# Performance work log

Measured on AMD Instinct MI355X. Metric: run time of the kernel, lower is better.

The kernel has to match this reference:

```python
import jax, jax.numpy as jnp
import numpy as np

N = 50000
E = 1600000
IN = 128
HID = 32
HEADS = 4
SLOPE = 0.2   # GATConv default negative_slope
EPS = 1e-5    # BatchNorm eps


def setup_inputs() -> dict:
    key = jax.random.key(0)
    ks = jax.random.split(key, 16)
    inp = {}
    inp["x"] = jax.random.normal(ks[0], (N, IN), dtype=jnp.float32)
    inp["edge_index"] = jax.random.randint(ks[1], (2, E), 0, N, dtype=jnp.int32)
    def p(k, shape, s=0.1):
        return jax.random.normal(k, shape, dtype=jnp.float32) * s
    # layer dims: (in_ch, out_ch_per_head, heads, concat)
    dims = [(IN, HID, HEADS, True), (HID * HEADS, HID, HEADS, True), (HID * HEADS, HID, 1, False)]
    i = 2
    for li, (ic, oc, h, concat) in enumerate(dims):
        inp[f"W{li}"] = p(ks[i], (ic, h * oc)); i += 1
        inp[f"as{li}"] = p(ks[i], (h, oc)); i += 1
        inp[f"ad{li}"] = p(ks[i], (h, oc)); i += 1
        bn_dim = h * oc if concat else oc
        inp[f"b{li}"] = jnp.zeros((bn_dim,), jnp.float32)
        inp[f"g{li}"] = jnp.ones((bn_dim,), jnp.float32)
        inp[f"be{li}"] = jnp.zeros((bn_dim,), jnp.float32)
    inp["cw1"] = p(ks[i], (HID, HID // 2)); i += 1
    inp["cb1"] = jnp.zeros((HID // 2,), jnp.float32)
    inp["cw2"] = p(ks[i], (HID // 2, 2)); i += 1
    inp["cb2"] = jnp.zeros((2,), jnp.float32)
    return inp


def _gat_layer(h, src, dst, W, a_s, a_d, b, heads, oc, concat):
    # PyG GATConv: x -> [N,H,C]; alpha = softmax_dst(leaky_relu(a_s.x_src + a_d.x_dst))
    n = h.shape[0]
    x = (h @ W).reshape(n, heads, oc)                 # [N,H,C]
    e_s = (x * a_s).sum(-1)                            # [N,H]
    e_d = (x * a_d).sum(-1)                            # [N,H]
    e = jax.nn.leaky_relu(e_s[src] + e_d[dst], SLOPE)  # [Etot,H]
    m = jax.ops.segment_max(e, dst, num_segments=n)    # segment softmax over dst
    ex = jnp.exp(e - m[dst])
    den = jax.ops.segment_sum(ex, dst, num_segments=n)
    alpha = ex / (den[dst] + 1e-16)                    # [Etot,H]
    out = jax.ops.segment_sum(x[src] * alpha[:, :, None], dst, num_segments=n)  # [N,H,C]
    out = out.reshape(n, heads * oc) if concat else out.mean(1)
    return out + b


def _bn(x, g, be):
    mu = x.mean(0)
    var = x.var(0)  # biased, as torch BN uses for normalization
    return g * (x - mu) * jax.lax.rsqrt(var + EPS) + be


def reference(x, edge_index, W0, as0, ad0, b0, g0, be0, W1, as1, ad1, b1, g1, be1,
              W2, as2, ad2, b2, g2, be2, cw1, cb1, cw2, cb2):
    n = x.shape[0]
    loops = jnp.arange(n, dtype=edge_index.dtype)      # add_self_loops=True default
    src = jnp.concatenate([edge_index[0], loops])
    dst = jnp.concatenate([edge_index[1], loops])
    layers = [(W0, as0, ad0, b0, g0, be0, HEADS, HID, True),
              (W1, as1, ad1, b1, g1, be1, HEADS, HID, True),
              (W2, as2, ad2, b2, g2, be2, 1, HID, False)]
    h = x
    for (W, a_s, a_d, b, g, be, heads, oc, concat) in layers:
        h = _gat_layer(h, src, dst, W, a_s, a_d, b, heads, oc, concat)
        h = jax.nn.elu(_bn(h, g, be))
    h = jax.nn.elu(h @ cw1 + cb1)
    return h @ cw2 + cb2
```

## Files before the change

### kernel.cpp

```cpp
#include <hip/hip_runtime.h>

static constexpr float SLOPE = 0.2f;
static constexpr float BN_EPS = 1e-5f;

static inline int cdiv(long long a, long long b) { return (int)((a + b - 1) / b); }

typedef __attribute__((ext_vector_type(8))) short short8;
typedef __attribute__((ext_vector_type(4))) float f32x4;

__device__ __forceinline__ unsigned short f2bf(float f) {
  unsigned u = __float_as_uint(f);
  u += 0x7fff + ((u >> 16) & 1);
  return (unsigned short)(u >> 16);
}
__device__ __forceinline__ float bf2f(unsigned short h) {
  return __uint_as_float((unsigned)h << 16);
}

static constexpr int EPB = 16384;

__global__ void csr_hist(const int* __restrict__ ei, int* __restrict__ counts,
                         int E, int NBLK, int NB) {
  __shared__ int cnt[256];
  const int tid = threadIdx.x;
  cnt[tid] = 0;
  __syncthreads();
  const int i0 = blockIdx.x * EPB;
  const int i1 = min(E, i0 + EPB);
  for (int i = i0 + tid; i < i1; i += 256) {
    int d = ei[E + i];
    atomicAdd(&cnt[d >> 8], 1);
  }
  __syncthreads();
  if (tid < NB) counts[tid * NBLK + blockIdx.x] = cnt[tid];
}

__global__ void csr_scan(const int* __restrict__ counts, int* __restrict__ offsets, int m) {
  __shared__ int wtot[16];
  __shared__ int woff[17];
  __shared__ int carry_sh;
  const int tid = threadIdx.x;
  const int lane = tid & 63;
  const int wv = tid >> 6;
  if (tid == 0) carry_sh = 0;
  __syncthreads();
  for (int base = 0; base < m; base += 1024) {
    int i = base + tid;
    int v = (i < m) ? counts[i] : 0;
    int x = v;
#pragma unroll
    for (int off = 1; off < 64; off <<= 1) {
      int y = __shfl_up(x, off);
      if (lane >= off) x += y;
    }
    if (lane == 63) wtot[wv] = x;
    __syncthreads();
    if (tid == 0) {
      int r = 0;
#pragma unroll
      for (int w = 0; w < 16; ++w) { woff[w] = r; r += wtot[w]; }
      woff[16] = r;
    }
    __syncthreads();
    if (i < m) offsets[i] = x - v + woff[wv] + carry_sh;
    __syncthreads();
    if (tid == 0) carry_sh += woff[16];
    __syncthreads();
  }
  if (tid == 0) offsets[m] = carry_sh;
}

__global__ void csr_part(const int* __restrict__ ei, const int* __restrict__ offsets,
                         unsigned* __restrict__ ebuf, int E, int NBLK, int NB) {
  __shared__ int cur[256];
  const int tid = threadIdx.x;
  cur[tid] = (tid < NB) ? offsets[tid * NBLK + blockIdx.x] : 0;
  __syncthreads();
  const int i0 = blockIdx.x * EPB;
  const int i1 = min(E, i0 + EPB);
  for (int i = i0 + tid; i < i1; i += 256) {
    int s = ei[i];
    int d = ei[E + i];
    int p = atomicAdd(&cur[d >> 8], 1);
    ebuf[p] = ((unsigned)s << 8) | (unsigned)(d & 255);
  }
}

__global__ void csr_bucket(const unsigned* __restrict__ ebuf, const int* __restrict__ offsets,
                           int* __restrict__ row_start, int* __restrict__ csr_src,
                           int n, int E, int NBLK, int NB) {
  __shared__ int nstart[256];
  __shared__ int wtot[4];
  const int b = blockIdx.x;
  const int base = b << 8;
  const int nn = min(256, n - base);
  const int estart = offsets[b * NBLK];
  const int eend = (b + 1 < NB) ? offsets[(b + 1) * NBLK] : E;
  const int gstart = estart + base;
  const int tid = threadIdx.x;
  nstart[tid] = (tid < nn) ? 1 : 0;
  __syncthreads();
  for (int j = estart + tid; j < eend; j += 256) {
    atomicAdd(&nstart[ebuf[j] & 255u], 1);
  }
  __syncthreads();
  const int lane = tid & 63, wv = tid >> 6;
  int v = nstart[tid];
  int x = v;
#pragma unroll
  for (int off = 1; off < 64; off <<= 1) {
    int y = __shfl_up(x, off);
    if (lane >= off) x += y;
  }
  if (lane == 63) wtot[wv] = x;
  __syncthreads();
  int add = 0;
  for (int w = 0; w < wv; ++w) add += wtot[w];
  int excl = x - v + add;
  __syncthreads();
  nstart[tid] = excl;
  if (tid < nn) row_start[base + tid] = gstart + excl;
  if (b == 0 && tid == 0) row_start[n] = E + n;
  __syncthreads();
  if (tid < nn) {
    int p = atomicAdd(&nstart[tid], 1);
    csr_src[gstart + p] = base + tid;
  }
  for (int j = estart + tid; j < eend; j += 256) {
    unsigned pk = ebuf[j];
    int p = atomicAdd(&nstart[pk & 255u], 1);
    csr_src[gstart + p] = (int)(pk >> 8);
  }
}

__global__ void wprep(const float* __restrict__ W0, const float* __restrict__ W1,
                      const float* __restrict__ W2,
                      unsigned short* __restrict__ Wt0, unsigned short* __restrict__ Wt1,
                      unsigned short* __restrict__ Wt2,
                      float* __restrict__ sums0, float* __restrict__ sums1,
                      float* __restrict__ sums2) {
  const int b = blockIdx.x;
  const int tid = threadIdx.x;
  if (b < 64) {
    int o = b * 256 + tid;
    int j = o >> 7, k = o & 127;
    Wt0[o] = f2bf(W0[k * 128 + j]);
  } else if (b < 128) {
    int o = (b - 64) * 256 + tid;
    int j = o >> 7, k = o & 127;
    Wt1[o] = f2bf(W1[k * 128 + j]);
  } else if (b < 144) {
    int o = (b - 128) * 256 + tid;
    int j = o >> 7, k = o & 127;
    Wt2[o] = f2bf(W2[k * 32 + j]);
  } else {
    sums0[tid] = 0.f;
    sums1[tid] = 0.f;
    if (tid < 64) sums2[tid] = 0.f;
  }
}

template<int IC, int OC, int H, bool BN, bool AF32>
__global__ void gemm_mfma(const unsigned short* __restrict__ Act,
                          const float* __restrict__ Axf,
                          const unsigned short* __restrict__ Wt,
                          const float* __restrict__ a_s, const float* __restrict__ a_d,
                          const float* __restrict__ bnsums, const float* __restrict__ g,
                          const float* __restrict__ be,
                          unsigned short* __restrict__ Pb, float* __restrict__ es,
                          float* __restrict__ ed, int n) {
  constexpr int NF = OC / 16;
  __shared__ float s_sc[IC], s_sf[IC];
  const int tid = threadIdx.x;
  if (BN) {
    const float inv_n = 1.f / (float)n;
    for (int c = tid; c < IC; c += 256) {
      float mu = bnsums[c] * inv_n;
      float var = bnsums[IC + c] * inv_n - mu * mu;
      float s = g[c] * rsqrtf(var + BN_EPS);
      s_sc[c] = s;
      s_sf[c] = be[c] - mu * s;
    }
    __syncthreads();
  }
  const int lane = tid & 63;
  const int l15 = lane & 15;
  const int lk = lane >> 4;
  const int node0 = blockIdx.x * 64 + (tid >> 6) * 16;
  const int arow = node0 + l15;
  const int ar = AF32 ? min(arow, n - 1) : arow;

  f32x4 acc[NF];
#pragma unroll
  for (int cb = 0; cb < NF; ++cb) acc[cb] = (f32x4){0.f, 0.f, 0.f, 0.f};

#pragma unroll
  for (int kc = 0; kc < IC / 32; ++kc) {
    const int kbase = kc * 32 + lk * 8;
    short8 a;
    if (AF32) {
      float4 u0 = *(const float4*)(Axf + (size_t)ar * IC + kbase);
      float4 u1 = *(const float4*)(Axf + (size_t)ar * IC + kbase + 4);
      a[0] = (short)f2bf(u0.x); a[1] = (short)f2bf(u0.y);
      a[2] = (short)f2bf(u0.z); a[3] = (short)f2bf(u0.w);
      a[4] = (short)f2bf(u1.x); a[5] = (short)f2bf(u1.y);
      a[6] = (short)f2bf(u1.z); a[7] = (short)f2bf(u1.w);
    } else {
      a = *(const short8*)(Act + (size_t)ar * IC + kbase);
    }
    if (BN) {
      short8 ta;
#pragma unroll
      for (int i = 0; i < 8; ++i) {
        float v = bf2f((unsigned short)a[i]);
        float y = fmaf(v, s_sc[kbase + i], s_sf[kbase + i]);
        y = (y > 0.f) ? y : (__expf(y) - 1.f);
        ta[i] = (short)f2bf(y);
      }
      a = ta;
    }
#pragma unroll
    for (int cb = 0; cb < NF; ++cb) {
      short8 b = *(const short8*)(Wt + (size_t)(cb * 16 + l15) * IC + kbase);
      acc[cb] = __builtin_amdgcn_mfma_f32_16x16x32_bf16(a, b, acc[cb], 0, 0, 0);
    }
  }

  float esum[4] = {0.f, 0.f, 0.f, 0.f}, edum[4] = {0.f, 0.f, 0.f, 0.f};
#pragma unroll
  for (int cb = 0; cb < NF; ++cb) {
    const int j = cb * 16 + l15;
    const float asv = a_s[j];
    const float adv = a_d[j];
#pragma unroll
    for (int i = 0; i < 4; ++i) {
      float p = acc[cb][i];
      int node = node0 + lk * 4 + i;
      if (node < n) Pb[(size_t)node * OC + j] = f2bf(p);
      float ps = p * asv, pd = p * adv;
#pragma unroll
      for (int mm = 1; mm <= 8; mm <<= 1) {
        ps += __shfl_xor(ps, mm);
        pd += __shfl_xor(pd, mm);
      }
      esum[i] += ps;
      edum[i] += pd;
    }
    if (cb & 1) {
      const int h = cb >> 1;
#pragma unroll
      for (int i = 0; i < 4; ++i) {
        int node = node0 + lk * 4 + i;
        if (l15 == 0 && node < n) {
          es[node * H + h] = esum[i];
          ed[node * H + h] = edum[i];
        }
        esum[i] = 0.f;
        edum[i] = 0.f;
      }
    }
  }
}

template<int H, int C>
__global__ void node_agg(const int* __restrict__ row_start, const int* __restrict__ csr_src,
                         const float* __restrict__ es, const float* __restrict__ ed,
                         const unsigned short* __restrict__ Pb, unsigned short* __restrict__ Ob,
                         int n) {
  constexpr int HC = H * C;
  constexpr int TPN = HC / 8;
  const int tid = threadIdx.x;
  const int t = tid % TPN;
  const int node = blockIdx.x * (256 / TPN) + tid / TPN;
  if (node >= n) return;
  const int h = (t * 8) / C;
  const int e0 = row_start[node];
  const int e1 = row_start[node + 1];
  const float edd = ed[node * H + h];
  const uint4* P4 = (const uint4*)Pb;
  float a0 = 0.f, a1 = 0.f, a2 = 0.f, a3 = 0.f;
  float a4 = 0.f, a5 = 0.f, a6 = 0.f, a7 = 0.f;
  float den = 0.f;
  int s0 = csr_src[e0];
  int s1 = (e0 + 1 < e1) ? csr_src[e0 + 1] : 0;
  int j = e0;
  while (j + 1 < e1) {
    const int nj = j + 2;
    int t0 = (nj < e1) ? csr_src[nj] : 0;
    int t1 = (nj + 1 < e1) ? csr_src[nj + 1] : 0;
    float x0 = es[s0 * H + h], x1 = es[s1 * H + h];
    uint4 p0 = P4[(size_t)s0 * TPN + t];
    uint4 p1 = P4[(size_t)s1 * TPN + t];
    x0 += edd; x0 = fmaxf(x0, SLOPE * x0); float w0 = __expf(x0);
    x1 += edd; x1 = fmaxf(x1, SLOPE * x1); float w1 = __expf(x1);
    den += w0 + w1;
    a0 = fmaf(w0, __uint_as_float(p0.x << 16), a0);
    a1 = fmaf(w0, __uint_as_float(p0.x & 0xffff0000u), a1);
    a2 = fmaf(w0, __uint_as_float(p0.y << 16), a2);
    a3 = fmaf(w0, __uint_as_float(p0.y & 0xffff0000u), a3);
    a4 = fmaf(w0, __uint_as_float(p0.z << 16), a4);
    a5 = fmaf(w0, __uint_as_float(p0.z & 0xffff0000u), a5);
    a6 = fmaf(w0, __uint_as_float(p0.w << 16), a6);
    a7 = fmaf(w0, __uint_as_float(p0.w & 0xffff0000u), a7);
    a0 = fmaf(w1, __uint_as_float(p1.x << 16), a0);
    a1 = fmaf(w1, __uint_as_float(p1.x & 0xffff0000u), a1);
    a2 = fmaf(w1, __uint_as_float(p1.y << 16), a2);
    a3 = fmaf(w1, __uint_as_float(p1.y & 0xffff0000u), a3);
    a4 = fmaf(w1, __uint_as_float(p1.z << 16), a4);
    a5 = fmaf(w1, __uint_as_float(p1.z & 0xffff0000u), a5);
    a6 = fmaf(w1, __uint_as_float(p1.w << 16), a6);
    a7 = fmaf(w1, __uint_as_float(p1.w & 0xffff0000u), a7);
    s0 = t0; s1 = t1; j = nj;
  }
  if (j < e1) {
    float x0 = es[s0 * H + h] + edd;
    x0 = fmaxf(x0, SLOPE * x0);
    float w0 = __expf(x0);
    den += w0;
    uint4 p0 = P4[(size_t)s0 * TPN + t];
    a0 = fmaf(w0, __uint_as_float(p0.x << 16), a0);
    a1 = fmaf(w0, __uint_as_float(p0.x & 0xffff0000u), a1);
    a2 = fmaf(w0, __uint_as_float(p0.y << 16), a2);
    a3 = fmaf(w0, __uint_as_float(p0.y & 0xffff0000u), a3);
    a4 = fmaf(w0, __uint_as_float(p0.z << 16), a4);
    a5 = fmaf(w0, __uint_as_float(p0.z & 0xffff0000u), a5);
    a6 = fmaf(w0, __uint_as_float(p0.w << 16), a6);
    a7 = fmaf(w0, __uint_as_float(p0.w & 0xffff0000u), a7);
  }
  float inv = 1.f / (den + 1e-16f);
  uint4 o;
  o.x = (unsigned)f2bf(a0 * inv) | ((unsigned)f2bf(a1 * inv) << 16);
  o.y = (unsigned)f2bf(a2 * inv) | ((unsigned)f2bf(a3 * inv) << 16);
  o.z = (unsigned)f2bf(a4 * inv) | ((unsigned)f2bf(a5 * inv) << 16);
  o.w = (unsigned)f2bf(a6 * inv) | ((unsigned)f2bf(a7 * inv) << 16);
  *(uint4*)(Ob + (size_t)node * HC + t * 8) = o;
}

template<int C>
__global__ void bn_stats2(const unsigned short* __restrict__ X, float* __restrict__ sums,
                          int n) {
  constexpr int TPR = C / 4;
  constexpr int RPB = 256 / TPR;
  __shared__ float ls[2 * C];
  const int tid = threadIdx.x;
  for (int i = tid; i < 2 * C; i += 256) ls[i] = 0.f;
  __syncthreads();
  const int c4 = (tid % TPR) * 4;
  const int rb = tid / TPR;
  float s0 = 0.f, s1 = 0.f, s2 = 0.f, s3 = 0.f;
  float q0 = 0.f, q1 = 0.f, q2 = 0.f, q3 = 0.f;
  for (int r = blockIdx.x * RPB + rb; r < n; r += gridDim.x * RPB) {
    uint2 v = *(const uint2*)(X + (size_t)r * C + c4);
    float f0 = __uint_as_float(v.x << 16);
    float f1 = __uint_as_float(v.x & 0xffff0000u);
    float f2 = __uint_as_float(v.y << 16);
    float f3 = __uint_as_float(v.y & 0xffff0000u);
    s0 += f0; q0 = fmaf(f0, f0, q0);
    s1 += f1; q1 = fmaf(f1, f1, q1);
    s2 += f2; q2 = fmaf(f2, f2, q2);
    s3 += f3; q3 = fmaf(f3, f3, q3);
  }
  atomicAdd(&ls[c4 + 0], s0);
  atomicAdd(&ls[c4 + 1], s1);
  atomicAdd(&ls[c4 + 2], s2);
  atomicAdd(&ls[c4 + 3], s3);
  atomicAdd(&ls[C + c4 + 0], q0);
  atomicAdd(&ls[C + c4 + 1], q1);
  atomicAdd(&ls[C + c4 + 2], q2);
  atomicAdd(&ls[C + c4 + 3], q3);
  __syncthreads();
  for (int i = tid; i < 2 * C; i += 256) unsafeAtomicAdd(&sums[i], ls[i]);
}

__global__ void mlp_head(const unsigned short* __restrict__ Hf, const float* __restrict__ bnsums,
                         const float* __restrict__ g, const float* __restrict__ be,
                         const float* __restrict__ cw1, const float* __restrict__ cb1,
                         const float* __restrict__ cw2, const float* __restrict__ cb2,
                         float* __restrict__ out, int n) {
  __shared__ float w1[32 * 16];
  __shared__ float b1[16];
  __shared__ float w2[16 * 2];
  __shared__ float b2[2];
  __shared__ float sc[32], sf[32];
  int tid = threadIdx.x;
  for (int i = tid; i < 32 * 16; i += blockDim.x) w1[i] = cw1[i];
  if (tid < 16) b1[tid] = cb1[tid];
  if (tid < 32) w2[tid] = cw2[tid];
  if (tid < 2) b2[tid] = cb2[tid];
  if (tid < 32) {
    float inv_n = 1.f / (float)n;
    float mu = bnsums[tid] * inv_n;
    float var = bnsums[32 + tid] * inv_n - mu * mu;
    float s = g[tid] * rsqrtf(var + BN_EPS);
    sc[tid] = s;
    sf[tid] = be[tid] - mu * s;
  }
  __syncthreads();
  int node = blockIdx.x * blockDim.x + tid;
  if (node >= n) return;
  float x[32];
  const uint4* xp = (const uint4*)(Hf + (size_t)node * 32);
#pragma unroll
  for (int q = 0; q < 4; ++q) {
    uint4 v = xp[q];
    unsigned pr[4] = {v.x, v.y, v.z, v.w};
#pragma unroll
    for (int u = 0; u < 4; ++u) {
      int c = q * 8 + u * 2;
      float va = __uint_as_float(pr[u] << 16);
      float vb = __uint_as_float(pr[u] & 0xffff0000u);
      float ya = fmaf(va, sc[c], sf[c]);
      float yb = fmaf(vb, sc[c + 1], sf[c + 1]);
      x[c] = (ya > 0.f) ? ya : (__expf(ya) - 1.f);
      x[c + 1] = (yb > 0.f) ? yb : (__expf(yb) - 1.f);
    }
  }
  float o0 = b2[0], o1 = b2[1];
#pragma unroll
  for (int j = 0; j < 16; ++j) {
    float acc = b1[j];
#pragma unroll
    for (int k = 0; k < 32; ++k) acc = fmaf(x[k], w1[k * 16 + j], acc);
    acc = (acc > 0.f) ? acc : (__expf(acc) - 1.f);
    o0 = fmaf(acc, w2[j * 2 + 0], o0);
    o1 = fmaf(acc, w2[j * 2 + 1], o1);
  }
  out[(size_t)node * 2 + 0] = o0;
  out[(size_t)node * 2 + 1] = o1;
}

extern "C" void kernel_launch(void* const* d_in, const int* in_sizes, int n_in,
                              void* d_out, int out_size, void* d_ws, size_t ws_size,
                              hipStream_t stream) {
  const float* x   = (const float*)d_in[0];
  const int*   ei  = (const int*)d_in[1];
  const float* W0  = (const float*)d_in[2];
  const float* as0 = (const float*)d_in[3];
  const float* ad0 = (const float*)d_in[4];
  const float* g0  = (const float*)d_in[6];
  const float* be0 = (const float*)d_in[7];
  const float* W1  = (const float*)d_in[8];
  const float* as1 = (const float*)d_in[9];
  const float* ad1 = (const float*)d_in[10];
  const float* g1  = (const float*)d_in[12];
  const float* be1 = (const float*)d_in[13];
  const float* W2  = (const float*)d_in[14];
  const float* as2 = (const float*)d_in[15];
  const float* ad2 = (const float*)d_in[16];
  const float* g2  = (const float*)d_in[18];
  const float* be2 = (const float*)d_in[19];
  const float* cw1 = (const float*)d_in[20];
  const float* cb1 = (const float*)d_in[21];
  const float* cw2 = (const float*)d_in[22];
  const float* cb2 = (const float*)d_in[23];

  const int n = in_sizes[0] / 128;
  const int E = in_sizes[1] / 2;
  const int n64 = cdiv(n, 64) * 64;

  const int NBLK = cdiv(E, EPB);
  const int NB = cdiv(n, 256);
  const int m = NB * NBLK;

  unsigned short* Ab  = (unsigned short*)d_ws;
  unsigned short* Bb  = Ab + (size_t)n64 * 128;
  unsigned short* Pb  = Bb + (size_t)n64 * 128;
  unsigned short* Af  = Pb + (size_t)n64 * 128;
  unsigned short* Wt0 = Af + (size_t)n64 * 32;
  unsigned short* Wt1 = Wt0 + 128 * 128;
  unsigned short* Wt2 = Wt1 + 128 * 128;
  float* es    = (float*)(Wt2 + 32 * 128);
  float* ed    = es + (size_t)n * 4;
  float* sums0 = ed + (size_t)n * 4;
  float* sums1 = sums0 + 256;
  float* sums2 = sums1 + 256;
  int* counts    = (int*)(sums2 + 64);
  int* offsets   = counts + m;
  int* row_start = offsets + m + 1;
  int* csr_src   = row_start + n + 1;
  unsigned* ebuf = (unsigned*)(csr_src + E + n);

  wprep<<<145, 256, 0, stream>>>(W0, W1, W2, Wt0, Wt1, Wt2, sums0, sums1, sums2);

  csr_hist<<<NBLK, 256, 0, stream>>>(ei, counts, E, NBLK, NB);
  csr_scan<<<1, 1024, 0, stream>>>(counts, offsets, m);
  csr_part<<<NBLK, 256, 0, stream>>>(ei, offsets, ebuf, E, NBLK, NB);
  csr_bucket<<<NB, 256, 0, stream>>>(ebuf, offsets, row_start, csr_src, n, E, NBLK, NB);

  gemm_mfma<128, 128, 4, false, true><<<cdiv(n, 64), 256, 0, stream>>>(
      nullptr, x, Wt0, as0, ad0, nullptr, nullptr, nullptr, Pb, es, ed, n);
  node_agg<4, 32><<<cdiv(n, 16), 256, 0, stream>>>(row_start, csr_src, es, ed, Pb, Ab, n);
  bn_stats2<128><<<1024, 256, 0, stream>>>(Ab, sums0, n);

  gemm_mfma<128, 128, 4, true, false><<<cdiv(n, 64), 256, 0, stream>>>(
      Ab, nullptr, Wt1, as1, ad1, sums0, g0, be0, Pb, es, ed, n);
  node_agg<4, 32><<<cdiv(n, 16), 256, 0, stream>>>(row_start, csr_src, es, ed, Pb, Bb, n);
  bn_stats2<128><<<1024, 256, 0, stream>>>(Bb, sums1, n);

  gemm_mfma<128, 32, 1, true, false><<<cdiv(n, 64), 256, 0, stream>>>(
      Bb, nullptr, Wt2, as2, ad2, sums1, g1, be1, Pb, es, ed, n);
  node_agg<1, 32><<<cdiv(n, 64), 256, 0, stream>>>(row_start, csr_src, es, ed, Pb, Af, n);
  bn_stats2<32><<<512, 256, 0, stream>>>(Af, sums2, n);

  mlp_head<<<cdiv(n, 256), 256, 0, stream>>>(Af, sums2, g2, be2, cw1, cb1, cw2, cb2,
                                             (float*)d_out, n);
}
```

Measured before the change: 412.1 us.

## Stage CSR scatter in LDS, fuse weight prep with histogram, unroll aggregation by four

```diff
diff --git a/kernel.cpp b/kernel.cpp
--- a/kernel.cpp
+++ b/kernel.cpp
@@ -17,130 +17,31 @@
   return __uint_as_float((unsigned)h << 16);
 }
 
-static constexpr int EPB = 16384;
-
-__global__ void csr_hist(const int* __restrict__ ei, int* __restrict__ counts,
-                         int E, int NBLK, int NB) {
-  __shared__ int cnt[256];
-  const int tid = threadIdx.x;
-  cnt[tid] = 0;
-  __syncthreads();
-  const int i0 = blockIdx.x * EPB;
-  const int i1 = min(E, i0 + EPB);
-  for (int i = i0 + tid; i < i1; i += 256) {
-    int d = ei[E + i];
-    atomicAdd(&cnt[d >> 8], 1);
-  }
-  __syncthreads();
-  if (tid < NB) counts[tid * NBLK + blockIdx.x] = cnt[tid];
-}
-
-__global__ void csr_scan(const int* __restrict__ counts, int* __restrict__ offsets, int m) {
-  __shared__ int wtot[16];
-  __shared__ int woff[17];
-  __shared__ int carry_sh;
-  const int tid = threadIdx.x;
-  const int lane = tid & 63;
-  const int wv = tid >> 6;
-  if (tid == 0) carry_sh = 0;
-  __syncthreads();
-  for (int base = 0; base < m; base += 1024) {
-    int i = base + tid;
-    int v = (i < m) ? counts[i] : 0;
-    int x = v;
-#pragma unroll
-    for (int off = 1; off < 64; off <<= 1) {
-      int y = __shfl_up(x, off);
-      if (lane >= off) x += y;
-    }
-    if (lane == 63) wtot[wv] = x;
+static constexpr int EPB = 8192;
+static constexpr int BCAP = 12288;
+
+__global__ void prep_hist(const int* __restrict__ ei, int* __restrict__ counts,
+                          const float* __restrict__ W0, const float* __restrict__ W1,
+                          const float* __restrict__ W2,
+                          unsigned short* __restrict__ Wt0, unsigned short* __restrict__ Wt1,
+                          unsigned short* __restrict__ Wt2,
+                          float* __restrict__ sums0, float* __restrict__ sums1,
+                          float* __restrict__ sums2,
+                          int E, int NBLK, int NB) {
+  const int tid = threadIdx.x;
+  const int blk = blockIdx.x;
+  if (blk < NBLK) {
+    __shared__ int cnt[256];
+    cnt[tid] = 0;
     __syncthreads();
-    if (tid == 0) {
-      int r = 0;
-#pragma unroll
-      for (int w = 0; w < 16; ++w) { woff[w] = r; r += wtot[w]; }
-      woff[16] = r;
-    }
+    const int i0 = blk * EPB;
+    const int i1 = min(E, i0 + EPB);
+    for (int i = i0 + tid; i < i1; i += 256) atomicAdd(&cnt[ei[E + i] >> 8], 1);
     __syncthreads();
-    if (i < m) offsets[i] = x - v + woff[wv] + carry_sh;
-    __syncthreads();
-    if (tid == 0) carry_sh += woff[16];
-    __syncthreads();
-  }
-  if (tid == 0) offsets[m] = carry_sh;
-}
-
-__global__ void csr_part(const int* __restrict__ ei, const int* __restrict__ offsets,
-                         unsigned* __restrict__ ebuf, int E, int NBLK, int NB) {
-  __shared__ int cur[256];
-  const int tid = threadIdx.x;
-  cur[tid] = (tid < NB) ? offsets[tid * NBLK + blockIdx.x] : 0;
-  __syncthreads();
-  const int i0 = blockIdx.x * EPB;
-  const int i1 = min(E, i0 + EPB);
-  for (int i = i0 + tid; i < i1; i += 256) {
-    int s = ei[i];
-    int d = ei[E + i];
-    int p = atomicAdd(&cur[d >> 8], 1);
-    ebuf[p] = ((unsigned)s << 8) | (unsigned)(d & 255);
-  }
-}
-
-__global__ void csr_bucket(const unsigned* __restrict__ ebuf, const int* __restrict__ offsets,
-                           int* __restrict__ row_start, int* __restrict__ csr_src,
-                           int n, int E, int NBLK, int NB) {
-  __shared__ int nstart[256];
-  __shared__ int wtot[4];
-  const int b = blockIdx.x;
-  const int base = b << 8;
-  const int nn = min(256, n - base);
-  const int estart = offsets[b * NBLK];
-  const int eend = (b + 1 < NB) ? offsets[(b + 1) * NBLK] : E;
-  const int gstart = estart + base;
-  const int tid = threadIdx.x;
-  nstart[tid] = (tid < nn) ? 1 : 0;
-  __syncthreads();
-  for (int j = estart + tid; j < eend; j += 256) {
-    atomicAdd(&nstart[ebuf[j] & 255u], 1);
-  }
-  __syncthreads();
-  const int lane = tid & 63, wv = tid >> 6;
-  int v = nstart[tid];
-  int x = v;
-#pragma unroll
-  for (int off = 1; off < 64; off <<= 1) {
-    int y = __shfl_up(x, off);
-    if (lane >= off) x += y;
-  }
-  if (lane == 63) wtot[wv] = x;
-  __syncthreads();
-  int add = 0;
-  for (int w = 0; w < wv; ++w) add += wtot[w];
-  int excl = x - v + add;
-  __syncthreads();
-  nstart[tid] = excl;
-  if (tid < nn) row_start[base + tid] = gstart + excl;
-  if (b == 0 && tid == 0) row_start[n] = E + n;
-  __syncthreads();
-  if (tid < nn) {
-    int p = atomicAdd(&nstart[tid], 1);
-    csr_src[gstart + p] = base + tid;
-  }
-  for (int j = estart + tid; j < eend; j += 256) {
-    unsigned pk = ebuf[j];
-    int p = atomicAdd(&nstart[pk & 255u], 1);
-    csr_src[gstart + p] = (int)(pk >> 8);
-  }
-}
-
-__global__ void wprep(const float* __restrict__ W0, const float* __restrict__ W1,
-                      const float* __restrict__ W2,
-                      unsigned short* __restrict__ Wt0, unsigned short* __restrict__ Wt1,
-                      unsigned short* __restrict__ Wt2,
-                      float* __restrict__ sums0, float* __restrict__ sums1,
-                      float* __restrict__ sums2) {
-  const int b = blockIdx.x;
-  const int tid = threadIdx.x;
+    if (tid < NB) counts[tid * NBLK + blk] = cnt[tid];
+    return;
+  }
+  const int b = blk - NBLK;
   if (b < 64) {
     int o = b * 256 + tid;
     int j = o >> 7, k = o & 127;
@@ -160,6 +61,127 @@
   }
 }
 
+__global__ void csr_scan2(const int* __restrict__ counts, int* __restrict__ offsets, int m) {
+  __shared__ int wtot[16];
+  const int tid = threadIdx.x;
+  const int lane = tid & 63, wv = tid >> 6;
+  const int CH = (m + 1023) >> 10;
+  const int lo = min(m, tid * CH);
+  const int hi = min(m, lo + CH);
+  int sum = 0;
+  for (int i = lo; i < hi; ++i) sum += counts[i];
+  int x = sum;
+#pragma unroll
+  for (int off = 1; off < 64; off <<= 1) {
+    int y = __shfl_up(x, off);
+    if (lane >= off) x += y;
+  }
+  if (lane == 63) wtot[wv] = x;
+  __syncthreads();
+  int add = 0;
+  for (int w = 0; w < wv; ++w) add += wtot[w];
+  int run = x - sum + add;
+  for (int i = lo; i < hi; ++i) { offsets[i] = run; run += counts[i]; }
+  if (hi == m) offsets[m] = run;
+}
+
+__global__ __launch_bounds__(256) void csr_part(const int* __restrict__ ei,
+                                                const int* __restrict__ offsets,
+                                                unsigned* __restrict__ ebuf,
+                                                int E, int NBLK, int NB) {
+  __shared__ unsigned stage[EPB];
+  __shared__ int cnt[256], sstart[256], cur[256], goff[256];
+  __shared__ int wtot[4];
+  const int tid = threadIdx.x;
+  const int blk = blockIdx.x;
+  const int lane = tid & 63, wv = tid >> 6;
+  cnt[tid] = 0;
+  if (tid < NB) goff[tid] = offsets[tid * NBLK + blk];
+  __syncthreads();
+  const int i0 = blk * EPB;
+  const int i1 = min(E, i0 + EPB);
+  for (int i = i0 + tid; i < i1; i += 256) atomicAdd(&cnt[ei[E + i] >> 8], 1);
+  __syncthreads();
+  int v = cnt[tid];
+  int x = v;
+#pragma unroll
+  for (int off = 1; off < 64; off <<= 1) {
+    int y = __shfl_up(x, off);
+    if (lane >= off) x += y;
+  }
+  if (lane == 63) wtot[wv] = x;
+  __syncthreads();
+  int add = 0;
+  for (int w = 0; w < wv; ++w) add += wtot[w];
+  int excl = x - v + add;
+  sstart[tid] = excl;
+  cur[tid] = excl;
+  __syncthreads();
+  for (int i = i0 + tid; i < i1; i += 256) {
+    int s = ei[i], d = ei[E + i];
+    int p = atomicAdd(&cur[d >> 8], 1);
+    stage[p] = ((unsigned)s << 8) | (unsigned)(d & 255);
+  }
+  __syncthreads();
+  for (int b = wv; b < NB; b += 4) {
+    const int ls = sstart[b], le = cur[b];
+    const int gbase = goff[b];
+    for (int e = ls + lane; e < le; e += 64) ebuf[gbase + (e - ls)] = stage[e];
+  }
+}
+
+__global__ __launch_bounds__(256) void csr_bucket(const unsigned* __restrict__ ebuf,
+                                                  const int* __restrict__ offsets,
+                                                  int* __restrict__ row_start,
+                                                  int* __restrict__ csr_src,
+                                                  int n, int E, int NBLK, int NB) {
+  __shared__ unsigned stage[BCAP];
+  __shared__ int deg[256], cur[256];
+  __shared__ int wtot[4];
+  const int b = blockIdx.x;
+  const int base = b << 8;
+  const int nn = min(256, n - base);
+  const int estart = offsets[b * NBLK];
+  const int eend = (b + 1 < NB) ? offsets[(b + 1) * NBLK] : E;
+  const int gstart = estart + base;
+  const int tid = threadIdx.x;
+  const int lane = tid & 63, wv = tid >> 6;
+  deg[tid] = (tid < nn) ? 1 : 0;
+  __syncthreads();
+  for (int j = estart + tid; j < eend; j += 256) atomicAdd(&deg[ebuf[j] & 255u], 1);
+  __syncthreads();
+  int v = deg[tid];
+  int x = v;
+#pragma unroll
+  for (int off = 1; off < 64; off <<= 1) {
+    int y = __shfl_up(x, off);
+    if (lane >= off) x += y;
+  }
+  if (lane == 63) wtot[wv] = x;
+  __syncthreads();
+  int add = 0;
+  for (int w = 0; w < wv; ++w) add += wtot[w];
+  int excl = x - v + add;
+  cur[tid] = excl;
+  if (tid < nn) row_start[base + tid] = gstart + excl;
+  if (b == 0 && tid == 0) row_start[n] = E + n;
+  __syncthreads();
+  if (tid < nn) {
+    int p = atomicAdd(&cur[tid], 1);
+    if (p < BCAP) stage[p] = (unsigned)(base + tid);
+    else csr_src[gstart + p] = base + tid;
+  }
+  for (int j = estart + tid; j < eend; j += 256) {
+    unsigned pk = ebuf[j];
+    int p = atomicAdd(&cur[pk & 255u], 1);
+    if (p < BCAP) stage[p] = pk >> 8;
+    else csr_src[gstart + p] = (int)(pk >> 8);
+  }
+  __syncthreads();
+  const int tot = min(eend - estart + nn, BCAP);
+  for (int e = tid; e < tot; e += 256) csr_src[gstart + e] = (int)stage[e];
+}
+
 template<int IC, int OC, int H, bool BN, bool AF32>
 __global__ void gemm_mfma(const unsigned short* __restrict__ Act,
                           const float* __restrict__ Axf,
@@ -282,18 +304,30 @@
   float a4 = 0.f, a5 = 0.f, a6 = 0.f, a7 = 0.f;
   float den = 0.f;
   int s0 = csr_src[e0];
-  int s1 = (e0 + 1 < e1) ? csr_src[e0 + 1] : 0;
-  int j = e0;
-  while (j + 1 < e1) {
-    const int nj = j + 2;
-    int t0 = (nj < e1) ? csr_src[nj] : 0;
-    int t1 = (nj + 1 < e1) ? csr_src[nj + 1] : 0;
+  int s1 = (e0 + 1 < e1) ? csr_src[e0 + 1] : s0;
+  int s2 = (e0 + 2 < e1) ? csr_src[e0 + 2] : s0;
+  int s3 = (e0 + 3 < e1) ? csr_src[e0 + 3] : s0;
+  for (int j = e0; j < e1; j += 4) {
+    const int nj = j + 4;
+    int t0 = (nj     < e1) ? csr_src[nj]     : s0;
+    int t1 = (nj + 1 < e1) ? csr_src[nj + 1] : s0;
+    int t2 = (nj + 2 < e1) ? csr_src[nj + 2] : s0;
+    int t3 = (nj + 3 < e1) ? csr_src[nj + 3] : s0;
     float x0 = es[s0 * H + h], x1 = es[s1 * H + h];
+    float x2 = es[s2 * H + h], x3 = es[s3 * H + h];
     uint4 p0 = P4[(size_t)s0 * TPN + t];
     uint4 p1 = P4[(size_t)s1 * TPN + t];
-    x0 += edd; x0 = fmaxf(x0, SLOPE * x0); float w0 = __expf(x0);
-    x1 += edd; x1 = fmaxf(x1, SLOPE * x1); float w1 = __expf(x1);
-    den += w0 + w1;
+    uint4 p2 = P4[(size_t)s2 * TPN + t];
+    uint4 p3 = P4[(size_t)s3 * TPN + t];
+    x0 += edd; x0 = fmaxf(x0, SLOPE * x0);
+    x1 += edd; x1 = fmaxf(x1, SLOPE * x1);
+    x2 += edd; x2 = fmaxf(x2, SLOPE * x2);
+    x3 += edd; x3 = fmaxf(x3, SLOPE * x3);
+    float w0 = __expf(x0);
+    float w1 = (j + 1 < e1) ? __expf(x1) : 0.f;
+    float w2 = (j + 2 < e1) ? __expf(x2) : 0.f;
+    float w3 = (j + 3 < e1) ? __expf(x3) : 0.f;
+    den += (w0 + w1) + (w2 + w3);
     a0 = fmaf(w0, __uint_as_float(p0.x << 16), a0);
     a1 = fmaf(w0, __uint_as_float(p0.x & 0xffff0000u), a1);
     a2 = fmaf(w0, __uint_as_float(p0.y << 16), a2);
@@ -310,22 +344,23 @@
     a5 = fmaf(w1, __uint_as_float(p1.z & 0xffff0000u), a5);
     a6 = fmaf(w1, __uint_as_float(p1.w << 16), a6);
     a7 = fmaf(w1, __uint_as_float(p1.w & 0xffff0000u), a7);
-    s0 = t0; s1 = t1; j = nj;
-  }
-  if (j < e1) {
-    float x0 = es[s0 * H + h] + edd;
-    x0 = fmaxf(x0, SLOPE * x0);
-    float w0 = __expf(x0);
-    den += w0;
-    uint4 p0 = P4[(size_t)s0 * TPN + t];
-    a0 = fmaf(w0, __uint_as_float(p0.x << 16), a0);
-    a1 = fmaf(w0, __uint_as_float(p0.x & 0xffff0000u), a1);
-    a2 = fmaf(w0, __uint_as_float(p0.y << 16), a2);
-    a3 = fmaf(w0, __uint_as_float(p0.y & 0xffff0000u), a3);
-    a4 = fmaf(w0, __uint_as_float(p0.z << 16), a4);
-    a5 = fmaf(w0, __uint_as_float(p0.z & 0xffff0000u), a5);
-    a6 = fmaf(w0, __uint_as_float(p0.w << 16), a6);
-    a7 = fmaf(w0, __uint_as_float(p0.w & 0xffff0000u), a7);
+    a0 = fmaf(w2, __uint_as_float(p2.x << 16), a0);
+    a1 = fmaf(w2, __uint_as_float(p2.x & 0xffff0000u), a1);
+    a2 = fmaf(w2, __uint_as_float(p2.y << 16), a2);
+    a3 = fmaf(w2, __uint_as_float(p2.y & 0xffff0000u), a3);
+    a4 = fmaf(w2, __uint_as_float(p2.z << 16), a4);
+    a5 = fmaf(w2, __uint_as_float(p2.z & 0xffff0000u), a5);
+    a6 = fmaf(w2, __uint_as_float(p2.w << 16), a6);
+    a7 = fmaf(w2, __uint_as_float(p2.w & 0xffff0000u), a7);
+    a0 = fmaf(w3, __uint_as_float(p3.x << 16), a0);
+    a1 = fmaf(w3, __uint_as_float(p3.x & 0xffff0000u), a1);
+    a2 = fmaf(w3, __uint_as_float(p3.y << 16), a2);
+    a3 = fmaf(w3, __uint_as_float(p3.y & 0xffff0000u), a3);
+    a4 = fmaf(w3, __uint_as_float(p3.z << 16), a4);
+    a5 = fmaf(w3, __uint_as_float(p3.z & 0xffff0000u), a5);
+    a6 = fmaf(w3, __uint_as_float(p3.w << 16), a6);
+    a7 = fmaf(w3, __uint_as_float(p3.w & 0xffff0000u), a7);
+    s0 = t0; s1 = t1; s2 = t2; s3 = t3;
   }
   float inv = 1.f / (den + 1e-16f);
   uint4 o;
@@ -480,10 +515,9 @@
   int* csr_src   = row_start + n + 1;
   unsigned* ebuf = (unsigned*)(csr_src + E + n);
 
-  wprep<<<145, 256, 0, stream>>>(W0, W1, W2, Wt0, Wt1, Wt2, sums0, sums1, sums2);
-
-  csr_hist<<<NBLK, 256, 0, stream>>>(ei, counts, E, NBLK, NB);
-  csr_scan<<<1, 1024, 0, stream>>>(counts, offsets, m);
+  prep_hist<<<NBLK + 145, 256, 0, stream>>>(ei, counts, W0, W1, W2, Wt0, Wt1, Wt2,
+                                            sums0, sums1, sums2, E, NBLK, NB);
+  csr_scan2<<<1, 1024, 0, stream>>>(counts, offsets, m);
   csr_part<<<NBLK, 256, 0, stream>>>(ei, offsets, ebuf, E, NBLK, NB);
   csr_bucket<<<NB, 256, 0, stream>>>(ebuf, offsets, row_start, csr_src, n, E, NBLK, NB);
 
```

Measured after the change: 424.6 us. +3.0%, slower.
